# Optimization experiments

Hardware: AMD Instinct MI355X
Metric: run time of the kernel (lower is better)

## Reference

```python
import jax, jax.numpy as jnp
import numpy as np

WS = 25          # window_size
THRESHOLD = 3.5  # default threshold in find_low_quality_regions


def _conv1d_gelu(x, w, b, pad):
    # x: (N, C_in, L), w: (C_out, C_in, K) -> gelu(conv(x) + b), SAME length
    y = jax.lax.conv_general_dilated(
        x, w, window_strides=(1,), padding=[(pad, pad)],
        dimension_numbers=("NCH", "OIH", "NCH"))
    return jax.nn.gelu(y + b[None, :, None], approximate=False)


def setup_inputs() -> dict:
    key = jax.random.key(0)
    ks = jax.random.split(key, 12)
    B, T, D, H = 8, 25000, 256, 128
    s = 0.05
    return {
        "latents": jax.random.normal(ks[0], (B, T, D), jnp.float32),
        "conv0_w": jax.random.normal(ks[1], (H, D, 7), jnp.float32) * s,
        "conv0_b": jax.random.normal(ks[2], (H,), jnp.float32) * s,
        "conv1_w": jax.random.normal(ks[3], (H, H, 5), jnp.float32) * s,
        "conv1_b": jax.random.normal(ks[4], (H,), jnp.float32) * s,
        "conv2_w": jax.random.normal(ks[5], (H, H, 5), jnp.float32) * s,
        "conv2_b": jax.random.normal(ks[6], (H,), jnp.float32) * s,
        "head_w1": jax.random.normal(ks[7], (H, H), jnp.float32) * s,
        "head_b1": jax.random.normal(ks[8], (H,), jnp.float32) * s,
        "head_w2": jax.random.normal(ks[9], (1, H), jnp.float32) * s,
        "head_b2": jax.random.normal(ks[10], (1,), jnp.float32) * s,
    }


def reference(latents, conv0_w, conv0_b, conv1_w, conv1_b, conv2_w, conv2_b,
              head_w1, head_b1, head_w2, head_b2):
    B, T, D = latents.shape
    nw = (T - WS) // WS + 1  # number of non-overlapping windows
    # (B, nw, WS, D) -> (B*nw, D, WS): batch all windows through the critic
    x = latents[:, :nw * WS].reshape(B, nw, WS, D).reshape(B * nw, WS, D)
    x = jnp.transpose(x, (0, 2, 1))  # NCH
    x = _conv1d_gelu(x, conv0_w, conv0_b, pad=3)
    x = _conv1d_gelu(x, conv1_w, conv1_b, pad=2)
    x = _conv1d_gelu(x, conv2_w, conv2_b, pad=2)
    feat = x.mean(axis=2)  # AdaptiveAvgPool1d(1) -> (B*nw, H)
    h = jax.nn.gelu(feat @ head_w1.T + head_b1, approximate=False)
    score = jax.nn.sigmoid(h @ head_w2.T + head_b2)[:, 0] * 5.0  # (B*nw,)
    scores = score.reshape(B, nw).mean(axis=0)  # critic(window).mean() per window
    low_quality = scores < THRESHOLD  # windows the loop would append as regions
    return scores, low_quality
```

## Files before the change

kernel.cpp:

```cpp
#include <hip/hip_runtime.h>
#include <math.h>

#define BATCH 8
#define T_LEN 25000
#define NW    1000
#define WS    25
#define D0    256
#define H     128

typedef __bf16 bf16;
typedef bf16 bf16x8 __attribute__((ext_vector_type(8)));
typedef bf16 bf16x4 __attribute__((ext_vector_type(4)));
typedef float f32x4 __attribute__((ext_vector_type(4)));

__device__ __forceinline__ float gelu_fast(float x) {
    float y = 0.7978845608f * x * (1.0f + 0.044715f * x * x);
    float e = __expf(2.0f * y);
    float t = 1.0f - 2.0f * __builtin_amdgcn_rcpf(e + 1.0f);
    return 0.5f * x * (1.0f + t);
}

__device__ __forceinline__ void repack_one(const float* __restrict__ w,
                                           bf16* __restrict__ dst, int idx,
                                           int Cin, int K, int KSn) {
    int j    = idx & 7;
    int lane = (idx >> 3) & 63;
    int mt   = (idx >> 9) & 7;
    int ks   = (idx >> 12) % KSn;
    int k    = idx / (4096 * KSn);
    int co = mt * 16 + (lane & 15);
    int ci = ks * 32 + (lane >> 4) * 8 + j;
    dst[idx] = (bf16)w[(co * Cin + ci) * K + k];
}

__global__ void prep_kernel(const float* __restrict__ c0w, const float* __restrict__ c1w,
                            const float* __restrict__ c2w, const float* __restrict__ hw1,
                            bf16* __restrict__ p0, bf16* __restrict__ p1,
                            bf16* __restrict__ p2, bf16* __restrict__ hw1b) {
    int t = blockIdx.x * 256 + threadIdx.x;
    if (t < 229376) {
        repack_one(c0w, p0, t, 256, 7, 8);
    } else if (t < 311296) {
        repack_one(c1w, p1, t - 229376, 128, 5, 4);
    } else if (t < 393216) {
        repack_one(c2w, p2, t - 311296, 128, 5, 4);
    } else if (t < 409600) {
        int i = t - 393216;
        hw1b[i] = (bf16)hw1[i];
    }
}

#define XT_LD 264
#define A_LD  136
#define OFF_A2   33456
#define OFF_FEAT 70752
#define OFF_H    72800
#define SMEM_BYTES 74848

__global__ __launch_bounds__(512, 4)
void critic_kernel(const float* __restrict__ lat,
                   const bf16* __restrict__ p0, const float* __restrict__ b0,
                   const bf16* __restrict__ p1, const float* __restrict__ b1,
                   const bf16* __restrict__ p2, const float* __restrict__ b2,
                   const bf16* __restrict__ hw1b, const float* __restrict__ hb1,
                   const float* __restrict__ hw2, const float* __restrict__ hb2,
                   float* __restrict__ scores_tmp) {
    __shared__ __align__(16) char smem[SMEM_BYTES];
    bf16  (*xT)[XT_LD]  = (bf16(*)[XT_LD])smem;
    bf16  (*a1T)[A_LD]  = (bf16(*)[A_LD])smem;
    bf16  (*a2T)[A_LD]  = (bf16(*)[A_LD])(smem + OFF_A2);
    float* feat = (float*)(smem + OFF_FEAT);
    float* hbuf = (float*)(smem + OFF_H);

    const int tid = threadIdx.x;
    const int bx  = blockIdx.x;
    const int b   = bx / (NW / 4);
    const int wi  = bx % (NW / 4);
    const int w0  = 4 * wi;

    {
        const float4* src4 = (const float4*)(lat + ((size_t)b * T_LEN + (size_t)w0 * WS) * D0);
        #pragma unroll
        for (int it = 0; it < 13; ++it) {
            int g = tid + it * 512;
            if (g < 6400) {
                int l = g >> 6, c0 = (g & 63) * 4;
                int win = l / 25, lr = l - win * 25;
                int r = 31 * win + lr + 3;
                float4 v = src4[g];
                bf16x4 o = {(bf16)v.x, (bf16)v.y, (bf16)v.z, (bf16)v.w};
                *(bf16x4*)&xT[r][c0] = o;
            }
        }
        bf16x4 z4 = {};
        #pragma unroll
        for (int it = 0; it < 3; ++it) {
            int i = tid + it * 512;
            int rr = i >> 6, c0 = (i & 63) * 4;
            int j = rr / 6, t6 = rr - 6 * j;
            int r = 31 * j + ((t6 < 3) ? t6 : t6 + 25);
            *(bf16x4*)&xT[r][c0] = z4;
        }
    }
    __syncthreads();

    const int lane = tid & 63, wv = tid >> 6;
    const int win = wv & 3, mtg = wv >> 2;
    const int m = lane & 15, q = lane >> 4;
    const bf16* xb  = &xT[m][q * 8];
    const bf16* a1b = &a1T[m][q * 8];

    f32x4 acc[4][2] = {};
    {
        const bf16x8* A = (const bf16x8*)p0 + (size_t)mtg * 256 + lane;
        #pragma unroll
        for (int k = 0; k < 7; ++k) {
            #pragma unroll
            for (int ks = 0; ks < 8; ++ks) {
                int f = (k * 8 + ks) * 512;
                bf16x8 a0 = A[f], a1 = A[f + 64], a2 = A[f + 128], a3 = A[f + 192];
                const bf16* pB = xb + (k + 31 * win) * XT_LD + ks * 32;
                bf16x8 bb0 = *(const bf16x8*)(pB);
                bf16x8 bb1 = *(const bf16x8*)(pB + 16 * XT_LD);
                acc[0][0] = __builtin_amdgcn_mfma_f32_16x16x32_bf16(a0, bb0, acc[0][0], 0, 0, 0);
                acc[0][1] = __builtin_amdgcn_mfma_f32_16x16x32_bf16(a0, bb1, acc[0][1], 0, 0, 0);
                acc[1][0] = __builtin_amdgcn_mfma_f32_16x16x32_bf16(a1, bb0, acc[1][0], 0, 0, 0);
                acc[1][1] = __builtin_amdgcn_mfma_f32_16x16x32_bf16(a1, bb1, acc[1][1], 0, 0, 0);
                acc[2][0] = __builtin_amdgcn_mfma_f32_16x16x32_bf16(a2, bb0, acc[2][0], 0, 0, 0);
                acc[2][1] = __builtin_amdgcn_mfma_f32_16x16x32_bf16(a2, bb1, acc[2][1], 0, 0, 0);
                acc[3][0] = __builtin_amdgcn_mfma_f32_16x16x32_bf16(a3, bb0, acc[3][0], 0, 0, 0);
                acc[3][1] = __builtin_amdgcn_mfma_f32_16x16x32_bf16(a3, bb1, acc[3][1], 0, 0, 0);
            }
        }
    }
    __syncthreads();
    {
        bf16x4 z4 = {};
        #pragma unroll
        for (int it = 0; it < 2; ++it) {
            int i = tid + it * 512;
            int arr = i >> 9, rr = (i >> 5) & 15, c0 = (i & 31) * 4;
            int j = rr >> 2, t4 = rr & 3;
            int r = 29 * j + ((t4 < 2) ? t4 : t4 + 25);
            if (arr == 0) *(bf16x4*)&a1T[r][c0] = z4;
            else          *(bf16x4*)&a2T[r][c0] = z4;
        }
    }
    #pragma unroll
    for (int i = 0; i < 4; ++i) {
        int co0 = (mtg * 4 + i) * 16 + q * 4;
        f32x4 bv = *(const f32x4*)&b0[co0];
        #pragma unroll
        for (int nt = 0; nt < 2; ++nt) {
            int l = nt * 16 + m;
            if (l < 25) {
                bf16x4 v;
                #pragma unroll
                for (int r = 0; r < 4; ++r)
                    v[r] = (bf16)gelu_fast(acc[i][nt][r] + bv[r]);
                *(bf16x4*)&a1T[l + 2 + 29 * win][co0] = v;
            }
        }
    }
    __syncthreads();

    f32x4 c1[4][2] = {};
    {
        const bf16x8* A = (const bf16x8*)p1 + (size_t)mtg * 256 + lane;
        #pragma unroll
        for (int k = 0; k < 5; ++k) {
            #pragma unroll
            for (int ks = 0; ks < 4; ++ks) {
                int f = (k * 4 + ks) * 512;
                bf16x8 a0 = A[f], a1 = A[f + 64], a2 = A[f + 128], a3 = A[f + 192];
                const bf16* pB = a1b + (k + 29 * win) * A_LD + ks * 32;
                bf16x8 bb0 = *(const bf16x8*)(pB);
                bf16x8 bb1 = *(const bf16x8*)(pB + 16 * A_LD);
                c1[0][0] = __builtin_amdgcn_mfma_f32_16x16x32_bf16(a0, bb0, c1[0][0], 0, 0, 0);
                c1[0][1] = __builtin_amdgcn_mfma_f32_16x16x32_bf16(a0, bb1, c1[0][1], 0, 0, 0);
                c1[1][0] = __builtin_amdgcn_mfma_f32_16x16x32_bf16(a1, bb0, c1[1][0], 0, 0, 0);
                c1[1][1] = __builtin_amdgcn_mfma_f32_16x16x32_bf16(a1, bb1, c1[1][1], 0, 0, 0);
                c1[2][0] = __builtin_amdgcn_mfma_f32_16x16x32_bf16(a2, bb0, c1[2][0], 0, 0, 0);
                c1[2][1] = __builtin_amdgcn_mfma_f32_16x16x32_bf16(a2, bb1, c1[2][1], 0, 0, 0);
                c1[3][0] = __builtin_amdgcn_mfma_f32_16x16x32_bf16(a3, bb0, c1[3][0], 0, 0, 0);
                c1[3][1] = __builtin_amdgcn_mfma_f32_16x16x32_bf16(a3, bb1, c1[3][1], 0, 0, 0);
            }
        }
    }
    #pragma unroll
    for (int i = 0; i < 4; ++i) {
        int co0 = (mtg * 4 + i) * 16 + q * 4;
        f32x4 bv = *(const f32x4*)&b1[co0];
        #pragma unroll
        for (int nt = 0; nt < 2; ++nt) {
            int l = nt * 16 + m;
            if (l < 25) {
                bf16x4 v;
                #pragma unroll
                for (int r = 0; r < 4; ++r)
                    v[r] = (bf16)gelu_fast(c1[i][nt][r] + bv[r]);
                *(bf16x4*)&a2T[l + 2 + 29 * win][co0] = v;
            }
        }
    }
    __syncthreads();

    f32x4 c2[4][2] = {};
    {
        const bf16* a2b = &a2T[m][q * 8];
        const bf16x8* A = (const bf16x8*)p2 + (size_t)mtg * 256 + lane;
        #pragma unroll
        for (int k = 0; k < 5; ++k) {
            #pragma unroll
            for (int ks = 0; ks < 4; ++ks) {
                int f = (k * 4 + ks) * 512;
                bf16x8 a0 = A[f], a1 = A[f + 64], a2 = A[f + 128], a3 = A[f + 192];
                const bf16* pB = a2b + (k + 29 * win) * A_LD + ks * 32;
                bf16x8 bb0 = *(const bf16x8*)(pB);
                bf16x8 bb1 = *(const bf16x8*)(pB + 16 * A_LD);
                c2[0][0] = __builtin_amdgcn_mfma_f32_16x16x32_bf16(a0, bb0, c2[0][0], 0, 0, 0);
                c2[0][1] = __builtin_amdgcn_mfma_f32_16x16x32_bf16(a0, bb1, c2[0][1], 0, 0, 0);
                c2[1][0] = __builtin_amdgcn_mfma_f32_16x16x32_bf16(a1, bb0, c2[1][0], 0, 0, 0);
                c2[1][1] = __builtin_amdgcn_mfma_f32_16x16x32_bf16(a1, bb1, c2[1][1], 0, 0, 0);
                c2[2][0] = __builtin_amdgcn_mfma_f32_16x16x32_bf16(a2, bb0, c2[2][0], 0, 0, 0);
                c2[2][1] = __builtin_amdgcn_mfma_f32_16x16x32_bf16(a2, bb1, c2[2][1], 0, 0, 0);
                c2[3][0] = __builtin_amdgcn_mfma_f32_16x16x32_bf16(a3, bb0, c2[3][0], 0, 0, 0);
                c2[3][1] = __builtin_amdgcn_mfma_f32_16x16x32_bf16(a3, bb1, c2[3][1], 0, 0, 0);
            }
        }
    }
    #pragma unroll
    for (int i = 0; i < 4; ++i) {
        int co0 = (mtg * 4 + i) * 16 + q * 4;
        f32x4 bv = *(const f32x4*)&b2[co0];
        f32x4 pool;
        #pragma unroll
        for (int r = 0; r < 4; ++r) {
            float s  = gelu_fast(c2[i][0][r] + bv[r]);
            float g1 = gelu_fast(c2[i][1][r] + bv[r]);
            s += (m < 9) ? g1 : 0.0f;
            s += __shfl_xor(s, 1);
            s += __shfl_xor(s, 2);
            s += __shfl_xor(s, 4);
            s += __shfl_xor(s, 8);
            pool[r] = s * 0.04f;
        }
        if (m == 0) *(f32x4*)&feat[win * 128 + co0] = pool;
    }
    __syncthreads();

    {
        int wb = tid >> 7, co = tid & 127;
        const bf16x8* row = (const bf16x8*)(hw1b + co * H);
        const float* f0 = feat + wb * 128;
        float a0h = hb1[co];
        #pragma unroll
        for (int jv = 0; jv < 16; ++jv) {
            bf16x8 w8 = row[jv];
            #pragma unroll
            for (int u = 0; u < 8; ++u)
                a0h += (float)w8[u] * f0[jv * 8 + u];
        }
        hbuf[wb * 128 + co] = gelu_fast(a0h);
    }
    __syncthreads();

    if (tid < 256) {
        int win2 = tid >> 6, j = tid & 63;
        const float* hb = hbuf + win2 * 128;
        float p = hw2[j] * hb[j] + hw2[j + 64] * hb[j + 64];
        #pragma unroll
        for (int off = 32; off > 0; off >>= 1) p += __shfl_down(p, off);
        if (j == 0) {
            float z = p + hb2[0];
            scores_tmp[b * NW + w0 + win2] = 5.0f / (1.0f + expf(-z));
        }
    }
}

__global__ void finalize_kernel(const float* __restrict__ tmp, float* __restrict__ out) {
    int w = blockIdx.x * 256 + threadIdx.x;
    if (w < NW) {
        float s = 0.0f;
        #pragma unroll
        for (int b = 0; b < BATCH; ++b) s += tmp[b * NW + w];
        s *= 0.125f;
        out[w] = s;
        out[NW + w] = (s < 3.5f) ? 1.0f : 0.0f;
    }
}

extern "C" void kernel_launch(void* const* d_in, const int* in_sizes, int n_in,
                              void* d_out, int out_size, void* d_ws, size_t ws_size,
                              hipStream_t stream) {
    const float* lat  = (const float*)d_in[0];
    const float* c0w  = (const float*)d_in[1];
    const float* c0b  = (const float*)d_in[2];
    const float* c1w  = (const float*)d_in[3];
    const float* c1b  = (const float*)d_in[4];
    const float* c2w  = (const float*)d_in[5];
    const float* c2b  = (const float*)d_in[6];
    const float* hw1  = (const float*)d_in[7];
    const float* hb1  = (const float*)d_in[8];
    const float* hw2  = (const float*)d_in[9];
    const float* hb2  = (const float*)d_in[10];

    bf16* p0   = (bf16*)d_ws;
    bf16* p1   = (bf16*)((char*)d_ws + 458752);
    bf16* p2   = (bf16*)((char*)d_ws + 622592);
    bf16* hw1b = (bf16*)((char*)d_ws + 786432);
    float* tmp = (float*)((char*)d_ws + 819200);

    prep_kernel<<<1600, 256, 0, stream>>>(c0w, c1w, c2w, hw1, p0, p1, p2, hw1b);
    critic_kernel<<<BATCH * (NW / 4), 512, 0, stream>>>(lat, p0, c0b, p1, c1b, p2, c2b,
                                                        hw1b, hb1, hw2, hb2, tmp);
    finalize_kernel<<<4, 256, 0, stream>>>(tmp, (float*)d_out);
}
```

Before: 526.6 us.

## Software-pipeline conv weight and LDS loads, prefetching weights across barriers

Replaces the three conv MFMA loops with a templated routine that keeps a three-stage register ring for weight loads from global memory and double-buffers the LDS activation reads one step ahead. The first two weight stages are issued before the preceding __syncthreads, so global weight latency overlaps the barrier and the previous stage's epilogue. This targets exposed load latency in front of each MFMA group, at the cost of more vector registers, which could spill or hurt occupancy under the 512x4 launch bound.

```diff
diff --git a/kernel.cpp b/kernel.cpp
--- a/kernel.cpp
+++ b/kernel.cpp
@@ -57,6 +57,49 @@
 #define OFF_H    72800
 #define SMEM_BYTES 74848
 
+template<int NS, int KSN, int LD>
+__device__ __forceinline__ void conv_phase(const bf16x8* __restrict__ A,
+                                           const bf16* __restrict__ bbase,
+                                           int rowoff, f32x4 (&acc)[4][2]) {
+    bf16x8 a[3][4];
+    bf16x8 bb[2][2];
+    #pragma unroll
+    for (int u = 0; u < 4; ++u) a[0][u] = A[u * 64];
+    #pragma unroll
+    for (int u = 0; u < 4; ++u) a[1][u] = A[512 + u * 64];
+    __syncthreads();
+    {
+        const bf16* pB = bbase + rowoff * LD;
+        bb[0][0] = *(const bf16x8*)pB;
+        bb[0][1] = *(const bf16x8*)(pB + 16 * LD);
+    }
+    #pragma unroll
+    for (int s = 0; s < NS; ++s) {
+        const int cur = s & 1, nxt = cur ^ 1;
+        const int ap = s % 3;
+        if (s + 2 < NS) {
+            const int ai = (s + 2) % 3;
+            const int f = (s + 2) * 512;
+            #pragma unroll
+            for (int u = 0; u < 4; ++u) a[ai][u] = A[f + u * 64];
+        }
+        if (s + 1 < NS) {
+            const int k1 = (s + 1) / KSN, ks1 = (s + 1) % KSN;
+            const bf16* pB = bbase + (k1 + rowoff) * LD + ks1 * 32;
+            bb[nxt][0] = *(const bf16x8*)pB;
+            bb[nxt][1] = *(const bf16x8*)(pB + 16 * LD);
+        }
+        acc[0][0] = __builtin_amdgcn_mfma_f32_16x16x32_bf16(a[ap][0], bb[cur][0], acc[0][0], 0, 0, 0);
+        acc[0][1] = __builtin_amdgcn_mfma_f32_16x16x32_bf16(a[ap][0], bb[cur][1], acc[0][1], 0, 0, 0);
+        acc[1][0] = __builtin_amdgcn_mfma_f32_16x16x32_bf16(a[ap][1], bb[cur][0], acc[1][0], 0, 0, 0);
+        acc[1][1] = __builtin_amdgcn_mfma_f32_16x16x32_bf16(a[ap][1], bb[cur][1], acc[1][1], 0, 0, 0);
+        acc[2][0] = __builtin_amdgcn_mfma_f32_16x16x32_bf16(a[ap][2], bb[cur][0], acc[2][0], 0, 0, 0);
+        acc[2][1] = __builtin_amdgcn_mfma_f32_16x16x32_bf16(a[ap][2], bb[cur][1], acc[2][1], 0, 0, 0);
+        acc[3][0] = __builtin_amdgcn_mfma_f32_16x16x32_bf16(a[ap][3], bb[cur][0], acc[3][0], 0, 0, 0);
+        acc[3][1] = __builtin_amdgcn_mfma_f32_16x16x32_bf16(a[ap][3], bb[cur][1], acc[3][1], 0, 0, 0);
+    }
+}
+
 __global__ __launch_bounds__(512, 4)
 void critic_kernel(const float* __restrict__ lat,
                    const bf16* __restrict__ p0, const float* __restrict__ b0,
@@ -102,7 +145,6 @@
             *(bf16x4*)&xT[r][c0] = z4;
         }
     }
-    __syncthreads();
 
     const int lane = tid & 63, wv = tid >> 6;
     const int win = wv & 3, mtg = wv >> 2;
@@ -111,28 +153,8 @@
     const bf16* a1b = &a1T[m][q * 8];
 
     f32x4 acc[4][2] = {};
-    {
-        const bf16x8* A = (const bf16x8*)p0 + (size_t)mtg * 256 + lane;
-        #pragma unroll
-        for (int k = 0; k < 7; ++k) {
-            #pragma unroll
-            for (int ks = 0; ks < 8; ++ks) {
-                int f = (k * 8 + ks) * 512;
-                bf16x8 a0 = A[f], a1 = A[f + 64], a2 = A[f + 128], a3 = A[f + 192];
-                const bf16* pB = xb + (k + 31 * win) * XT_LD + ks * 32;
-                bf16x8 bb0 = *(const bf16x8*)(pB);
-                bf16x8 bb1 = *(const bf16x8*)(pB + 16 * XT_LD);
-                acc[0][0] = __builtin_amdgcn_mfma_f32_16x16x32_bf16(a0, bb0, acc[0][0], 0, 0, 0);
-                acc[0][1] = __builtin_amdgcn_mfma_f32_16x16x32_bf16(a0, bb1, acc[0][1], 0, 0, 0);
-                acc[1][0] = __builtin_amdgcn_mfma_f32_16x16x32_bf16(a1, bb0, acc[1][0], 0, 0, 0);
-                acc[1][1] = __builtin_amdgcn_mfma_f32_16x16x32_bf16(a1, bb1, acc[1][1], 0, 0, 0);
-                acc[2][0] = __builtin_amdgcn_mfma_f32_16x16x32_bf16(a2, bb0, acc[2][0], 0, 0, 0);
-                acc[2][1] = __builtin_amdgcn_mfma_f32_16x16x32_bf16(a2, bb1, acc[2][1], 0, 0, 0);
-                acc[3][0] = __builtin_amdgcn_mfma_f32_16x16x32_bf16(a3, bb0, acc[3][0], 0, 0, 0);
-                acc[3][1] = __builtin_amdgcn_mfma_f32_16x16x32_bf16(a3, bb1, acc[3][1], 0, 0, 0);
-            }
-        }
-    }
+    conv_phase<56, 8, XT_LD>((const bf16x8*)p0 + (size_t)mtg * 256 + lane,
+                             xb, 31 * win, acc);
     __syncthreads();
     {
         bf16x4 z4 = {};
@@ -162,31 +184,10 @@
             }
         }
     }
-    __syncthreads();
 
     f32x4 c1[4][2] = {};
-    {
-        const bf16x8* A = (const bf16x8*)p1 + (size_t)mtg * 256 + lane;
-        #pragma unroll
-        for (int k = 0; k < 5; ++k) {
-            #pragma unroll
-            for (int ks = 0; ks < 4; ++ks) {
-                int f = (k * 4 + ks) * 512;
-                bf16x8 a0 = A[f], a1 = A[f + 64], a2 = A[f + 128], a3 = A[f + 192];
-                const bf16* pB = a1b + (k + 29 * win) * A_LD + ks * 32;
-                bf16x8 bb0 = *(const bf16x8*)(pB);
-                bf16x8 bb1 = *(const bf16x8*)(pB + 16 * A_LD);
-                c1[0][0] = __builtin_amdgcn_mfma_f32_16x16x32_bf16(a0, bb0, c1[0][0], 0, 0, 0);
-                c1[0][1] = __builtin_amdgcn_mfma_f32_16x16x32_bf16(a0, bb1, c1[0][1], 0, 0, 0);
-                c1[1][0] = __builtin_amdgcn_mfma_f32_16x16x32_bf16(a1, bb0, c1[1][0], 0, 0, 0);
-                c1[1][1] = __builtin_amdgcn_mfma_f32_16x16x32_bf16(a1, bb1, c1[1][1], 0, 0, 0);
-                c1[2][0] = __builtin_amdgcn_mfma_f32_16x16x32_bf16(a2, bb0, c1[2][0], 0, 0, 0);
-                c1[2][1] = __builtin_amdgcn_mfma_f32_16x16x32_bf16(a2, bb1, c1[2][1], 0, 0, 0);
-                c1[3][0] = __builtin_amdgcn_mfma_f32_16x16x32_bf16(a3, bb0, c1[3][0], 0, 0, 0);
-                c1[3][1] = __builtin_amdgcn_mfma_f32_16x16x32_bf16(a3, bb1, c1[3][1], 0, 0, 0);
-            }
-        }
-    }
+    conv_phase<20, 4, A_LD>((const bf16x8*)p1 + (size_t)mtg * 256 + lane,
+                            a1b, 29 * win, c1);
     #pragma unroll
     for (int i = 0; i < 4; ++i) {
         int co0 = (mtg * 4 + i) * 16 + q * 4;
@@ -203,32 +204,10 @@
             }
         }
     }
-    __syncthreads();
 
     f32x4 c2[4][2] = {};
-    {
-        const bf16* a2b = &a2T[m][q * 8];
-        const bf16x8* A = (const bf16x8*)p2 + (size_t)mtg * 256 + lane;
-        #pragma unroll
-        for (int k = 0; k < 5; ++k) {
-            #pragma unroll
-            for (int ks = 0; ks < 4; ++ks) {
-                int f = (k * 4 + ks) * 512;
-                bf16x8 a0 = A[f], a1 = A[f + 64], a2 = A[f + 128], a3 = A[f + 192];
-                const bf16* pB = a2b + (k + 29 * win) * A_LD + ks * 32;
-                bf16x8 bb0 = *(const bf16x8*)(pB);
-                bf16x8 bb1 = *(const bf16x8*)(pB + 16 * A_LD);
-                c2[0][0] = __builtin_amdgcn_mfma_f32_16x16x32_bf16(a0, bb0, c2[0][0], 0, 0, 0);
-                c2[0][1] = __builtin_amdgcn_mfma_f32_16x16x32_bf16(a0, bb1, c2[0][1], 0, 0, 0);
-                c2[1][0] = __builtin_amdgcn_mfma_f32_16x16x32_bf16(a1, bb0, c2[1][0], 0, 0, 0);
-                c2[1][1] = __builtin_amdgcn_mfma_f32_16x16x32_bf16(a1, bb1, c2[1][1], 0, 0, 0);
-                c2[2][0] = __builtin_amdgcn_mfma_f32_16x16x32_bf16(a2, bb0, c2[2][0], 0, 0, 0);
-                c2[2][1] = __builtin_amdgcn_mfma_f32_16x16x32_bf16(a2, bb1, c2[2][1], 0, 0, 0);
-                c2[3][0] = __builtin_amdgcn_mfma_f32_16x16x32_bf16(a3, bb0, c2[3][0], 0, 0, 0);
-                c2[3][1] = __builtin_amdgcn_mfma_f32_16x16x32_bf16(a3, bb1, c2[3][1], 0, 0, 0);
-            }
-        }
-    }
+    conv_phase<20, 4, A_LD>((const bf16x8*)p2 + (size_t)mtg * 256 + lane,
+                            &a2T[m][q * 8], 29 * win, c2);
     #pragma unroll
     for (int i = 0; i < 4; ++i) {
         int co0 = (mtg * 4 + i) * 16 + q * 4;
```

Measured after the change: 511.0 us. 3.0% less time.
